# Optimization experiments

Measured on AMD Instinct MI355X. Metric: run time of the kernel, lower is better.

Reference implementation:

```python
import jax, jax.numpy as jnp
import numpy as np

THRESHOLD = 0.1
N_HEAD = 16
NEG_INF = -1e9


def setup_inputs() -> dict:
    key = jax.random.key(0)
    ks = jax.random.split(key, 8)
    B, T, C = 2, 2048, 1024
    H, D, R = N_HEAD, C // N_HEAD, 8
    return {
        "x": jax.random.normal(ks[0], (B, T, C), dtype=jnp.float32),
        "W_attn": jax.random.normal(ks[1], (C, 3 * C), dtype=jnp.float32) * 0.02,
        "W_proj": jax.random.normal(ks[2], (C, C), dtype=jnp.float32) * 0.02,
        "W_recip": jax.random.normal(ks[3], (D, R), dtype=jnp.float32) * 0.02,
        "w_std": jax.random.uniform(ks[4], (H,), dtype=jnp.float32),
        "w_rec": jax.random.uniform(ks[5], (H,), dtype=jnp.float32),
        "w_disc": jax.random.uniform(ks[6], (H,), dtype=jnp.float32),
        "d_bias": jax.random.normal(ks[7], (H, T), dtype=jnp.float32) * 0.02,
    }


def reference(x, W_attn, W_proj, W_recip, w_std, w_rec, w_disc, d_bias):
    B, T, C = x.shape
    H = N_HEAD
    D = C // H
    R = W_recip.shape[1]
    D_std = D - R

    # QKV projection (Linear without bias)
    qkv = x @ W_attn  # [B,T,3C]
    q, k, v = jnp.split(qkv, 3, axis=2)

    def to_heads(t):
        return t.reshape(B, T, H, D).transpose(0, 2, 1, 3)  # [B,H,T,D]

    q, k, v = to_heads(q), to_heads(k), to_heads(v)

    # low-rank reciprocal projections
    QW = q @ W_recip  # [B,H,T,R]
    KW = k @ W_recip

    ws = jnp.sqrt(jnp.clip(w_std, 1e-8))[:, None, None]  # [H,1,1]
    wr = jnp.sqrt(jnp.clip(w_rec, 1e-8))[:, None, None]
    use_ra = (w_rec > THRESHOLD)[:, None, None]  # [H,1,1]

    # RA heads: augmented Q/K = [ws*Q_std | wr*KW] / [ws*K_std | wr*QW]
    q_aug = jnp.concatenate([ws * q[..., :D_std], wr * KW], axis=-1)
    k_aug = jnp.concatenate([ws * k[..., :D_std], wr * QW], axis=-1)
    q_eff = jnp.where(use_ra, q_aug, ws * q)
    k_eff = jnp.where(use_ra, k_aug, ws * k)

    # mean-centered discoverability column bias: [1,H,1,T]
    d = d_bias[:, :T]
    d = d - d.mean(axis=-1, keepdims=True)
    bias = (d * w_disc[:, None])[None, :, None, :]

    scale = 1.0 / jnp.sqrt(jnp.asarray(D, dtype=x.dtype))
    scores = jnp.einsum("bhid,bhjd->bhij", q_eff, k_eff) * scale + bias
    causal = jnp.tril(jnp.ones((T, T), dtype=bool))
    scores = jnp.where(causal[None, None], scores, NEG_INF)
    attn = jax.nn.softmax(scores, axis=-1)
    out = jnp.einsum("bhij,bhjd->bhid", attn, v)  # [B,H,T,D]

    out = out.transpose(0, 2, 1, 3).reshape(B, T, C)
    return out @ W_proj
```

## Files before the change

### kernel.cpp

```cpp
#include <hip/hip_runtime.h>
#include <hip/hip_bf16.h>

#define DEVI __device__ __forceinline__

typedef __attribute__((ext_vector_type(8))) short short8;
typedef __attribute__((ext_vector_type(4))) short short4v;
typedef __attribute__((ext_vector_type(4))) float floatx4;

static constexpr int B_ = 2, T_ = 2048, C_ = 1024, H_ = 16, D_ = 64;
static constexpr float LOG2E = 1.44269504088896f;

DEVI float bf2f(unsigned short u) {
    union { unsigned int i; float f; } v; v.i = ((unsigned int)u) << 16; return v.f;
}
DEVI unsigned short f2bf(float f) {
    union { float f; unsigned int i; } v; v.f = f;
    unsigned int x = v.i;
    return (unsigned short)((x + 0x7fffu + ((x >> 16) & 1u)) >> 16);
}
DEVI unsigned int pk2bf(float lo, float hi) {
#if __has_builtin(__builtin_amdgcn_cvt_pk_bf16_f32)
    typedef __attribute__((ext_vector_type(2))) __bf16 bf16x2;
    union { bf16x2 v; unsigned int u; } r;
    r.v = __builtin_amdgcn_cvt_pk_bf16_f32(lo, hi);
    return r.u;
#else
    return (unsigned int)f2bf(lo) | ((unsigned int)f2bf(hi) << 16);
#endif
}
DEVI float fast_exp2(float x) {
#if __has_builtin(__builtin_amdgcn_exp2f)
    return __builtin_amdgcn_exp2f(x);
#else
    return __expf(x * 0.6931471805599453f);
#endif
}

DEVI void async16(const unsigned short* g, unsigned short* l) {
    __builtin_amdgcn_global_load_lds((const __attribute__((address_space(1))) void*)g,
                                     (__attribute__((address_space(3))) void*)l, 16, 0, 0);
}

DEVI void tr_body(const float* in, unsigned short* out, int K, int N, int bx, int by,
                  int tid, float (*tile)[65], float scale, bool skiphi) {
    int k0 = by * 64, n0 = bx * 64;
#pragma unroll
    for (int r = 0; r < 4; r++) {
        int ci = tid + r * 256;
        int row = ci >> 4, c4 = (ci & 15) * 4;
        float4 v = *(const float4*)&in[(size_t)(k0 + row) * N + n0 + c4];
        tile[row][c4 + 0] = v.x; tile[row][c4 + 1] = v.y;
        tile[row][c4 + 2] = v.z; tile[row][c4 + 3] = v.w;
    }
    __syncthreads();
#pragma unroll
    for (int r = 0; r < 2; r++) {
        int ci = tid + r * 256;
        int row = ci >> 3, c8 = (ci & 7) * 8;
        if (skiphi && row >= 56) continue;
        union { unsigned short u[8]; short8 s; } o;
#pragma unroll
        for (int j = 0; j < 8; j++) o.u[j] = f2bf(tile[c8 + j][row] * scale);
        *(short8*)&out[(size_t)(n0 + row) * K + k0 + c8] = o.s;
    }
}

__global__ __launch_bounds__(256) void k_prep(const float* __restrict__ x,
                                              const float* __restrict__ W_attn,
                                              const float* __restrict__ W_proj,
                                              const float* __restrict__ d_bias,
                                              const float* __restrict__ w_disc,
                                              const float* __restrict__ W_recip,
                                              const float* __restrict__ w_std,
                                              const float* __restrict__ w_rec,
                                              unsigned short* __restrict__ x_bf,
                                              unsigned short* __restrict__ wa_t,
                                              unsigned short* __restrict__ wp_t,
                                              float* __restrict__ bias) {
    __shared__ float tile[64][65];
    __shared__ float red[256];
    int bid = blockIdx.x, tid = threadIdx.x;
    if (bid < 2048) {
        int i = bid * 256 + tid;
        const float4* p = (const float4*)x + (size_t)i * 2;
        float4 a = p[0], b = p[1];
        union { unsigned short u[8]; short8 s; } r;
        r.u[0] = f2bf(a.x); r.u[1] = f2bf(a.y); r.u[2] = f2bf(a.z); r.u[3] = f2bf(a.w);
        r.u[4] = f2bf(b.x); r.u[5] = f2bf(b.y); r.u[6] = f2bf(b.z); r.u[7] = f2bf(b.w);
        *(short8*)&x_bf[(size_t)i * 8] = r.s;
    } else if (bid < 2816) {
        int idx = bid - 2048;
        int bx = idx % 48, by = idx / 48;
        int sec = bx >> 4, h = bx & 15;
        float ws = sqrtf(fmaxf(w_std[h], 1e-8f));
        float sc = (sec == 0) ? ws * (0.125f * LOG2E) : (sec == 1 ? ws : 1.0f);
        tr_body(W_attn, wa_t, 1024, 3072, bx, by, tid, tile, sc, sec < 2);
    } else if (bid < 3072) {
        int idx = bid - 2816;
        tr_body(W_proj, wp_t, 1024, 1024, idx & 15, idx >> 4, tid, tile, 1.0f, false);
    } else if (bid < 3088) {
        int h = bid - 3072;
        float s = 0.f;
        for (int t = tid; t < T_; t += 256) s += d_bias[h * T_ + t];
        red[tid] = s;
        __syncthreads();
        for (int st = 128; st > 0; st >>= 1) {
            if (tid < st) red[tid] += red[tid + st];
            __syncthreads();
        }
        float mean = red[0] * (1.0f / T_);
        float wd = w_disc[h] * LOG2E;
        for (int t = tid; t < T_; t += 256) bias[h * T_ + t] = (d_bias[h * T_ + t] - mean) * wd;
    } else {
        int idx = bid - 3088;
        int h = idx & 15, side = idx >> 4;
        float* WrS = &tile[0][0];
        for (int i = tid; i < 512; i += 256) WrS[i] = W_recip[i];
        __syncthreads();
        float wrv = sqrtf(fmaxf(w_rec[h], 1e-8f));
        float wsv = sqrtf(fmaxf(w_std[h], 1e-8f));
        bool ra = w_rec[h] > 0.1f;
        float sc = (side == 0 ? 0.125f * LOG2E : 1.0f) * (ra ? wrv : wsv);
        int dst0 = side * 1024 + h * 64 + 56;
        for (int kk = tid; kk < 1024; kk += 256) {
            const float* srow = W_attn + (size_t)kk * 3072;
            float out[8];
            if (ra) {
                int sc0 = (1 - side) * 1024 + h * 64;
#pragma unroll
                for (int r = 0; r < 8; r++) out[r] = 0.f;
                for (int dd = 0; dd < 64; dd++) {
                    float v = srow[sc0 + dd];
#pragma unroll
                    for (int r = 0; r < 8; r++) out[r] += v * WrS[dd * 8 + r];
                }
            } else {
                int sc0 = side * 1024 + h * 64 + 56;
#pragma unroll
                for (int r = 0; r < 8; r++) out[r] = srow[sc0 + r];
            }
#pragma unroll
            for (int r = 0; r < 8; r++)
                wa_t[(size_t)(dst0 + r) * 1024 + kk] = f2bf(sc * out[r]);
        }
    }
}

__global__ __launch_bounds__(256) void k_gemm_qkv(const unsigned short* __restrict__ A,
                                                  const unsigned short* __restrict__ Bt,
                                                  unsigned short* __restrict__ qe,
                                                  unsigned short* __restrict__ ke,
                                                  unsigned short* __restrict__ vt,
                                                  int M, int N, int K) {
    __shared__ __align__(16) unsigned short As[128 * 32];
    __shared__ __align__(16) unsigned short Bs[128 * 32];
    __shared__ __align__(16) unsigned short stg[4][4096];
    int b1d = blockIdx.y * 24 + blockIdx.x;
    int xcd = b1d & 7, i6 = b1d >> 3;
    int bx = (xcd & 1) * 12 + i6 % 12;
    int by = (xcd >> 1) * 8 + i6 / 12;
    int m0 = by * 128, n0 = bx * 128;
    int tid = threadIdx.x, l = tid & 63, w = tid >> 6;
    int wm = (w >> 1) * 64, wn = (w & 1) * 64;
    int lm = l & 15, lq = l >> 4;
    floatx4 acc[4][4];
#pragma unroll
    for (int a = 0; a < 4; a++)
#pragma unroll
        for (int b = 0; b < 4; b++) acc[a][b] = {0.f, 0.f, 0.f, 0.f};

    for (int k0 = 0; k0 < K; k0 += 32) {
        __syncthreads();
#pragma unroll
        for (int r = 0; r < 2; r++) {
            int ci = tid + r * 256;
            int row = ci >> 2, off = (ci & 3) * 8;
            async16(&A[(size_t)(m0 + row) * K + k0 + off], &As[row * 32 + off]);
            async16(&Bt[(size_t)(n0 + row) * K + k0 + off], &Bs[row * 32 + off]);
        }
        __syncthreads();
        short8 af[4], bf[4];
#pragma unroll
        for (int t = 0; t < 4; t++) af[t] = *(short8*)&As[(wm + t * 16 + lm) * 32 + lq * 8];
#pragma unroll
        for (int t = 0; t < 4; t++) bf[t] = *(short8*)&Bs[(wn + t * 16 + lm) * 32 + lq * 8];
#pragma unroll
        for (int tm = 0; tm < 4; tm++)
#pragma unroll
            for (int tn = 0; tn < 4; tn++)
                acc[tm][tn] = __builtin_amdgcn_mfma_f32_16x16x32_bf16(af[tm], bf[tn], acc[tm][tn], 0, 0, 0);
    }
    int sec = bx >> 3;
    int b = by >> 4;
    int head = ((n0 & 1023) >> 6) + (wn >> 6);
    size_t bhbase = (size_t)(b * 16 + head) * 131072;
    int tloc0 = (m0 & 2047) + wm;
    unsigned short* dst = (sec == 0) ? qe : (sec == 1) ? ke : vt;
    unsigned short* S = stg[w];
    if (sec < 2) {
#pragma unroll
        for (int tm = 0; tm < 4; tm++)
#pragma unroll
            for (int tn = 0; tn < 4; tn++) {
                int base = tm * 1024 + (tn >> 1) * 512 + ((tn & 1) * 2 + (lm >> 3)) * 128 +
                           (lm & 7) + lq * 32;
#pragma unroll
                for (int r = 0; r < 4; r++) S[base + r * 8] = f2bf(acc[tm][tn][r]);
            }
    } else {
#pragma unroll
        for (int tm = 0; tm < 4; tm++)
#pragma unroll
            for (int tn = 0; tn < 4; tn++) {
                int base = (tm >> 1) * 2048 + tn * 512 + ((tm & 1) * 2 + (lq >> 1)) * 128 +
                           lm * 8 + (lq & 1) * 4;
                union { unsigned short u[4]; short4v s4; } o;
#pragma unroll
                for (int r = 0; r < 4; r++) o.u[r] = f2bf(acc[tm][tn][r]);
                *(short4v*)&S[base] = o.s4;
            }
    }
    size_t gbase = bhbase + ((sec < 2) ? (size_t)(tloc0 >> 4) * 1024
                                       : (size_t)(tloc0 >> 5) * 2048);
#pragma unroll
    for (int i = 0; i < 8; i++) {
        short8 v = *(const short8*)&S[(size_t)(i * 64 + l) * 8];
        *(short8*)&dst[gbase + (size_t)(i * 64 + l) * 8] = v;
    }
}

__global__ __launch_bounds__(256) void k_gemm64(const unsigned short* __restrict__ A,
                                                const unsigned short* __restrict__ Bt,
                                                float* __restrict__ C, int M, int N, int K) {
    __shared__ __align__(16) unsigned short As[128 * 32];
    __shared__ __align__(16) unsigned short Bs[64 * 32];
    int b1d = blockIdx.y * 16 + blockIdx.x;
    int xcd = b1d & 7, i6 = b1d >> 3;
    int bx = (xcd & 1) * 8 + (i6 & 7);
    int by = (xcd >> 1) * 8 + (i6 >> 3);
    int m0 = by * 128, n0 = bx * 64;
    int tid = threadIdx.x, l = tid & 63, w = tid >> 6;
    int wm = w * 32;
    int lm = l & 15, lq = l >> 4;
    floatx4 acc[2][4];
#pragma unroll
    for (int a = 0; a < 2; a++)
#pragma unroll
        for (int b = 0; b < 4; b++) acc[a][b] = {0.f, 0.f, 0.f, 0.f};

    for (int k0 = 0; k0 < K; k0 += 32) {
        __syncthreads();
#pragma unroll
        for (int r = 0; r < 2; r++) {
            int ci = tid + r * 256;
            int row = ci >> 2, off = (ci & 3) * 8;
            async16(&A[(size_t)(m0 + row) * K + k0 + off], &As[row * 32 + off]);
        }
        {
            int row = tid >> 2, off = (tid & 3) * 8;
            async16(&Bt[(size_t)(n0 + row) * K + k0 + off], &Bs[row * 32 + off]);
        }
        __syncthreads();
        short8 af[2], bf[4];
#pragma unroll
        for (int t = 0; t < 2; t++) af[t] = *(short8*)&As[(wm + t * 16 + lm) * 32 + lq * 8];
#pragma unroll
        for (int t = 0; t < 4; t++) bf[t] = *(short8*)&Bs[(t * 16 + lm) * 32 + lq * 8];
#pragma unroll
        for (int tm = 0; tm < 2; tm++)
#pragma unroll
            for (int tn = 0; tn < 4; tn++)
                acc[tm][tn] = __builtin_amdgcn_mfma_f32_16x16x32_bf16(af[tm], bf[tn], acc[tm][tn], 0, 0, 0);
    }
#pragma unroll
    for (int tm = 0; tm < 2; tm++)
#pragma unroll
        for (int tn = 0; tn < 4; tn++) {
            int row = m0 + wm + tm * 16 + lq * 4;
            int col = n0 + tn * 16 + lm;
#pragma unroll
            for (int r = 0; r < 4; r++) C[(size_t)(row + r) * N + col] = acc[tm][tn][r];
        }
}

DEVI void exp_pack(float sv[4][4], float& l_part, unsigned int pk[4][2]) {
#pragma unroll
    for (int js = 0; js < 4; js++)
#pragma unroll
        for (int r = 0; r < 4; r++) {
            float p = fast_exp2(sv[js][r]);
            sv[js][r] = p;
            l_part += p;
        }
#pragma unroll
    for (int js = 0; js < 4; js++) {
        pk[js][0] = pk2bf(sv[js][0], sv[js][1]);
        pk[js][1] = pk2bf(sv[js][2], sv[js][3]);
    }
}

DEVI short8 make_pf(const unsigned int pk[4][2], int c, int srcLo, int srcHi, bool hi) {
    int a0 = __shfl((int)pk[2 * c][0], srcLo);
    int a1 = __shfl((int)pk[2 * c][1], srcLo);
    int a2 = __shfl((int)pk[2 * c][0], srcHi);
    int a3 = __shfl((int)pk[2 * c][1], srcHi);
    int b0 = __shfl((int)pk[2 * c + 1][0], srcLo);
    int b1 = __shfl((int)pk[2 * c + 1][1], srcLo);
    int b2 = __shfl((int)pk[2 * c + 1][0], srcHi);
    int b3 = __shfl((int)pk[2 * c + 1][1], srcHi);
    union { int i[4]; short8 s; } pf;
    pf.i[0] = hi ? b0 : a0;
    pf.i[1] = hi ? b1 : a1;
    pf.i[2] = hi ? b2 : a2;
    pf.i[3] = hi ? b3 : a3;
    return pf.s;
}

struct KF { short8 lo[4]; short8 hi[4]; };

__global__ __launch_bounds__(256) void k_attn(const unsigned short* __restrict__ qe,
                                              const unsigned short* __restrict__ ke,
                                              const unsigned short* __restrict__ vt,
                                              const float* __restrict__ bias,
                                              unsigned short* __restrict__ obf) {
    int b1d = blockIdx.y * 16 + blockIdx.x;
    int xcd = b1d & 7, j = b1d >> 3;
    int bh = xcd * 4 + (j >> 4);
    int px = j & 15;
    int b = bh >> 4, h = bh & 15;
    int tid = threadIdx.x, l = tid & 63, w = tid >> 6;
    int lm = l & 15, lq = l >> 4;
    int l8 = l * 8;
    const size_t hb = (size_t)bh * 131072;
    const unsigned short* qeh = qe + hb;
    const unsigned short* keh = ke + hb;
    const unsigned short* vth = vt + hb;
    const float* biash = bias + h * T_;

    int gA = px * 4 + w;
    int gB = 127 - gA;
    int itA = (gA >> 2) + 1, itB = (gB >> 2) + 1;
    int irowA = gA * 16 + lm, irowB = gB * 16 + lm;

    short8 qA0 = *(const short8*)(qeh + (size_t)gA * 1024 + l8);
    short8 qA1 = *(const short8*)(qeh + (size_t)gA * 1024 + 512 + l8);
    short8 qB0 = *(const short8*)(qeh + (size_t)gB * 1024 + l8);
    short8 qB1 = *(const short8*)(qeh + (size_t)gB * 1024 + 512 + l8);

    floatx4 OA[4], OB[4];
#pragma unroll
    for (int i = 0; i < 4; i++) { OA[i] = {0.f, 0.f, 0.f, 0.f}; OB[i] = {0.f, 0.f, 0.f, 0.f}; }
    float lA = 0.f, lB = 0.f;

    const int srcLo = ((lq & 1) * 2) * 16 + lm;
    const int srcHi = srcLo + 16;
    const bool hi = (lq >> 1) & 1;

    KF kfa, kfb;
#pragma unroll
    for (int js = 0; js < 4; js++) {
        const unsigned short* kp = keh + (size_t)js * 1024 + l8;
        kfa.lo[js] = *(const short8*)kp;
        kfa.hi[js] = *(const short8*)(kp + 512);
    }

    auto step = [&](int s, KF& cur, KF& nxt) {
        int j0 = s * 64;
        bool doA = (s < itA);
        bool maskA = (s == itA - 1);
        bool maskB = (s == itB - 1);
        {
            const unsigned short* kb = keh + (size_t)(s + 1) * 4096 + l8;
#pragma unroll
            for (int js = 0; js < 4; js++) {
                nxt.lo[js] = *(const short8*)(kb + js * 1024);
                nxt.hi[js] = *(const short8*)(kb + js * 1024 + 512);
            }
        }
        short8 vfr[2][4];
#pragma unroll
        for (int c = 0; c < 2; c++)
#pragma unroll
            for (int dt = 0; dt < 4; dt++)
                vfr[c][dt] = *(const short8*)(vth + (size_t)((j0 >> 5) + c) * 2048 + dt * 512 + l8);
        float bv[4][4];
#pragma unroll
        for (int js = 0; js < 4; js++) {
            float4 bj = *(const float4*)&biash[j0 + js * 16 + lq * 4];
            bv[js][0] = bj.x; bv[js][1] = bj.y; bv[js][2] = bj.z; bv[js][3] = bj.w;
        }
        floatx4 sb4[4], sa4[4];
#pragma unroll
        for (int js = 0; js < 4; js++) {
            floatx4 sb = {0.f, 0.f, 0.f, 0.f};
            sb = __builtin_amdgcn_mfma_f32_16x16x32_bf16(cur.lo[js], qB0, sb, 0, 0, 0);
            sb = __builtin_amdgcn_mfma_f32_16x16x32_bf16(cur.hi[js], qB1, sb, 0, 0, 0);
            sb4[js] = sb;
        }
        if (doA) {
#pragma unroll
            for (int js = 0; js < 4; js++) {
                floatx4 sa = {0.f, 0.f, 0.f, 0.f};
                sa = __builtin_amdgcn_mfma_f32_16x16x32_bf16(cur.lo[js], qA0, sa, 0, 0, 0);
                sa = __builtin_amdgcn_mfma_f32_16x16x32_bf16(cur.hi[js], qA1, sa, 0, 0, 0);
                sa4[js] = sa;
            }
        }
        float svB[4][4];
#pragma unroll
        for (int js = 0; js < 4; js++)
#pragma unroll
            for (int r = 0; r < 4; r++) svB[js][r] = sb4[js][r] + bv[js][r];
        if (maskB) {
#pragma unroll
            for (int js = 0; js < 4; js++) {
                int jb = j0 + js * 16 + lq * 4;
#pragma unroll
                for (int r = 0; r < 4; r++)
                    if (jb + r > irowB) svB[js][r] = -1e9f;
            }
        }
        unsigned int pkB[4][2];
        exp_pack(svB, lB, pkB);

        if (doA) {
            float svA[4][4];
#pragma unroll
            for (int js = 0; js < 4; js++)
#pragma unroll
                for (int r = 0; r < 4; r++) svA[js][r] = sa4[js][r] + bv[js][r];
            if (maskA) {
#pragma unroll
                for (int js = 0; js < 4; js++) {
                    int jb = j0 + js * 16 + lq * 4;
#pragma unroll
                    for (int r = 0; r < 4; r++)
                        if (jb + r > irowA) svA[js][r] = -1e9f;
                }
            }
            unsigned int pkA[4][2];
            exp_pack(svA, lA, pkA);
#pragma unroll
            for (int c = 0; c < 2; c++) {
                short8 pfA = make_pf(pkA, c, srcLo, srcHi, hi);
                short8 pfB = make_pf(pkB, c, srcLo, srcHi, hi);
#pragma unroll
                for (int dt = 0; dt < 4; dt++) {
                    OA[dt] = __builtin_amdgcn_mfma_f32_16x16x32_bf16(vfr[c][dt], pfA, OA[dt], 0, 0, 0);
                    OB[dt] = __builtin_amdgcn_mfma_f32_16x16x32_bf16(vfr[c][dt], pfB, OB[dt], 0, 0, 0);
                }
            }
        } else {
#pragma unroll
            for (int c = 0; c < 2; c++) {
                short8 pfB = make_pf(pkB, c, srcLo, srcHi, hi);
#pragma unroll
                for (int dt = 0; dt < 4; dt++)
                    OB[dt] = __builtin_amdgcn_mfma_f32_16x16x32_bf16(vfr[c][dt], pfB, OB[dt], 0, 0, 0);
            }
        }
    };

    int s = 0;
    for (; s + 2 <= itB; s += 2) {
        step(s, kfa, kfb);
        step(s + 1, kfb, kfa);
    }
    if (s < itB) step(s, kfa, kfb);

    lA += __shfl_xor(lA, 16); lA += __shfl_xor(lA, 32);
    lB += __shfl_xor(lB, 16); lB += __shfl_xor(lB, 32);
    {
        float inv = 1.0f / lA;
        unsigned short* orow = obf + (size_t)(b * T_ + irowA) * C_ + h * 64;
#pragma unroll
        for (int dt = 0; dt < 4; dt++) {
            union { unsigned short u[4]; short4v s4; } o;
#pragma unroll
            for (int r = 0; r < 4; r++) o.u[r] = f2bf(OA[dt][r] * inv);
            *(short4v*)&orow[dt * 16 + lq * 4] = o.s4;
        }
    }
    {
        float inv = 1.0f / lB;
        unsigned short* orow = obf + (size_t)(b * T_ + irowB) * C_ + h * 64;
#pragma unroll
        for (int dt = 0; dt < 4; dt++) {
            union { unsigned short u[4]; short4v s4; } o;
#pragma unroll
            for (int r = 0; r < 4; r++) o.u[r] = f2bf(OB[dt][r] * inv);
            *(short4v*)&orow[dt * 16 + lq * 4] = o.s4;
        }
    }
}

extern "C" void kernel_launch(void* const* d_in, const int* in_sizes, int n_in,
                              void* d_out, int out_size, void* d_ws, size_t ws_size,
                              hipStream_t stream) {
    const float* x       = (const float*)d_in[0];
    const float* W_attn  = (const float*)d_in[1];
    const float* W_proj  = (const float*)d_in[2];
    const float* W_recip = (const float*)d_in[3];
    const float* w_std   = (const float*)d_in[4];
    const float* w_rec   = (const float*)d_in[5];
    const float* w_disc  = (const float*)d_in[6];
    const float* d_bias  = (const float*)d_in[7];

    char* ws = (char*)d_ws;
    size_t o = 0;
    unsigned short* x_bf = (unsigned short*)(ws + o); o += (size_t)4096 * 1024 * 2;
    unsigned short* wa_t = (unsigned short*)(ws + o); o += (size_t)3072 * 1024 * 2;
    unsigned short* wp_t = (unsigned short*)(ws + o); o += (size_t)1024 * 1024 * 2;
    unsigned short* qe   = (unsigned short*)(ws + o); o += (size_t)32 * 2048 * 64 * 2;
    unsigned short* ke   = (unsigned short*)(ws + o); o += (size_t)32 * 2048 * 64 * 2;
    unsigned short* vt   = (unsigned short*)(ws + o); o += (size_t)32 * 2048 * 64 * 2;
    unsigned short* obf  = (unsigned short*)(ws + o); o += (size_t)4096 * 1024 * 2;
    float* bias          = (float*)(ws + o);          o += (size_t)16 * 2048 * 4;

    k_prep<<<3120, 256, 0, stream>>>(x, W_attn, W_proj, d_bias, w_disc, W_recip, w_std, w_rec,
                                     x_bf, wa_t, wp_t, bias);
    k_gemm_qkv<<<dim3(24, 32), 256, 0, stream>>>(x_bf, wa_t, qe, ke, vt, 4096, 3072, 1024);
    k_attn<<<dim3(16, 32), 256, 0, stream>>>(qe, ke, vt, bias, obf);
    k_gemm64<<<dim3(16, 32), 256, 0, stream>>>(obf, wp_t, (float*)d_out, 4096, 1024, 1024);
}
```

Baseline: 204.4 us.

## Split attention KV loop across two waves per query pair and reduce via LDS

```diff
diff --git a/kernel.cpp b/kernel.cpp
--- a/kernel.cpp
+++ b/kernel.cpp
@@ -323,12 +323,15 @@
                                               const unsigned short* __restrict__ vt,
                                               const float* __restrict__ bias,
                                               unsigned short* __restrict__ obf) {
-    int b1d = blockIdx.y * 16 + blockIdx.x;
+    __shared__ __align__(16) float psum[2][64][36];
+    int b1d = blockIdx.y * 32 + blockIdx.x;
     int xcd = b1d & 7, j = b1d >> 3;
-    int bh = xcd * 4 + (j >> 4);
-    int px = j & 15;
+    int bh = xcd * 4 + (j >> 5);
+    int pxq = j & 31;
     int b = bh >> 4, h = bh & 15;
     int tid = threadIdx.x, l = tid & 63, w = tid >> 6;
+    int pairL = w >> 1;
+    int phase = w & 1;
     int lm = l & 15, lq = l >> 4;
     int l8 = l * 8;
     const size_t hb = (size_t)bh * 131072;
@@ -337,7 +340,7 @@
     const unsigned short* vth = vt + hb;
     const float* biash = bias + h * T_;
 
-    int gA = px * 4 + w;
+    int gA = pxq * 2 + pairL;
     int gB = 127 - gA;
     int itA = (gA >> 2) + 1, itB = (gB >> 2) + 1;
     int irowA = gA * 16 + lm, irowB = gB * 16 + lm;
@@ -359,7 +362,7 @@
     KF kfa, kfb;
 #pragma unroll
     for (int js = 0; js < 4; js++) {
-        const unsigned short* kp = keh + (size_t)js * 1024 + l8;
+        const unsigned short* kp = keh + (size_t)phase * 4096 + (size_t)js * 1024 + l8;
         kfa.lo[js] = *(const short8*)kp;
         kfa.hi[js] = *(const short8*)(kp + 512);
     }
@@ -370,7 +373,7 @@
         bool maskA = (s == itA - 1);
         bool maskB = (s == itB - 1);
         {
-            const unsigned short* kb = keh + (size_t)(s + 1) * 4096 + l8;
+            const unsigned short* kb = keh + (size_t)(s + 2) * 4096 + l8;
 #pragma unroll
             for (int js = 0; js < 4; js++) {
                 nxt.lo[js] = *(const short8*)(kb + js * 1024);
@@ -461,12 +464,32 @@
         }
     };
 
-    int s = 0;
-    for (; s + 2 <= itB; s += 2) {
+    int s = phase;
+    for (; s + 2 < itB; s += 4) {
         step(s, kfa, kfb);
-        step(s + 1, kfb, kfa);
+        step(s + 2, kfb, kfa);
     }
     if (s < itB) step(s, kfa, kfb);
+
+    if (phase == 1) {
+        float* dst = psum[pairL][l];
+#pragma unroll
+        for (int dt = 0; dt < 4; dt++) *(floatx4*)&dst[dt * 4] = OA[dt];
+#pragma unroll
+        for (int dt = 0; dt < 4; dt++) *(floatx4*)&dst[16 + dt * 4] = OB[dt];
+        dst[32] = lA; dst[33] = lB;
+    }
+    __syncthreads();
+    if (phase == 1) return;
+    {
+        const float* src = psum[pairL][l];
+#pragma unroll
+        for (int dt = 0; dt < 4; dt++) {
+            OA[dt] += *(const floatx4*)&src[dt * 4];
+            OB[dt] += *(const floatx4*)&src[16 + dt * 4];
+        }
+        lA += src[32]; lB += src[33];
+    }
 
     lA += __shfl_xor(lA, 16); lA += __shfl_xor(lA, 32);
     lB += __shfl_xor(lB, 16); lB += __shfl_xor(lB, 32);
@@ -520,6 +543,6 @@
     k_prep<<<3120, 256, 0, stream>>>(x, W_attn, W_proj, d_bias, w_disc, W_recip, w_std, w_rec,
                                      x_bf, wa_t, wp_t, bias);
     k_gemm_qkv<<<dim3(24, 32), 256, 0, stream>>>(x_bf, wa_t, qe, ke, vt, 4096, 3072, 1024);
-    k_attn<<<dim3(16, 32), 256, 0, stream>>>(qe, ke, vt, bias, obf);
+    k_attn<<<dim3(32, 32), 256, 0, stream>>>(qe, ke, vt, bias, obf);
     k_gemm64<<<dim3(16, 32), 256, 0, stream>>>(obf, wp_t, (float*)d_out, 4096, 1024, 1024);
 }
```

Measured after the change: 204.7 us. Within noise of the previous version (+0.2%).
